# Performance work log

Measured on AMD Instinct MI355X. Metric: run time of the kernel, lower is better.

## Reference

```python
import jax, jax.numpy as jnp
import numpy as np

TEMPERATURE = 0.5
EPS = 1e-8  # matches torch cosine_similarity eps guard semantics (norm clamp)


def setup_inputs() -> dict:
    key = jax.random.key(0)
    k1, k2 = jax.random.split(key)
    B, D = 4096, 256
    z_i = jax.random.normal(k1, (B, D), dtype=jnp.float32)
    z_j = jax.random.normal(k2, (B, D), dtype=jnp.float32)
    return {"z_i": z_i, "z_j": z_j}


def reference(z_i, z_j):
    B = z_i.shape[0]
    z = jnp.concatenate([z_i, z_j], axis=0)            # [2B, D]
    # cosine similarity: normalize once, then GEMM
    norm = jnp.maximum(jnp.linalg.norm(z, axis=1, keepdims=True), EPS)
    zn = z / norm                                       # [2B, D]
    sim = zn @ zn.T                                     # [2B, 2B]
    # positives: diag(sim, +B) and diag(sim, -B)
    idx = jnp.arange(B)
    sim_ij = sim[idx, idx + B]
    sim_ji = sim[idx + B, idx]
    positives = jnp.concatenate([sim_ij, sim_ji])       # [2B]
    # masked denominator: exclude self-similarity
    mask = 1.0 - jnp.eye(2 * B, dtype=sim.dtype)
    denom = jnp.sum(mask * jnp.exp(sim / TEMPERATURE), axis=1)  # [2B]
    all_losses = -jnp.log(jnp.exp(positives / TEMPERATURE) / denom)
    return jnp.sum(all_losses) / (2 * B)
```

## Files before the change

### kernel.cpp

```cpp
#include <hip/hip_runtime.h>
#include <hip/hip_bf16.h>
#include <cstdint>
#include <cstddef>
#include <math.h>

#define D 256
#define TEMP_INV 2.0f
#define EPS_NORM 1e-8f
#define NTILES 2080

typedef __attribute__((ext_vector_type(8))) short bf16x8;
typedef __attribute__((ext_vector_type(4))) float f32x4;

__global__ void __launch_bounds__(256) normalize_rows(
    const float* __restrict__ zi, const float* __restrict__ zj,
    __hip_bfloat16* __restrict__ zn, float* __restrict__ out, int B) {
  const int wid = threadIdx.x >> 6;
  const int lane = threadIdx.x & 63;
  if (blockIdx.x == 0 && threadIdx.x == 0) out[0] = 0.0f;
#pragma unroll
  for (int it = 0; it < 4; ++it) {
    int row = it * 2048 + blockIdx.x * 4 + wid;
    const float* src = (row < B) ? (zi + (size_t)row * D)
                                 : (zj + (size_t)(row - B) * D);
    float4 v = ((const float4*)src)[lane];
    float ss = v.x * v.x + v.y * v.y + v.z * v.z + v.w * v.w;
    for (int off = 32; off; off >>= 1) ss += __shfl_xor(ss, off);
    float rn = 1.0f / fmaxf(sqrtf(ss), EPS_NORM);
    union { ushort4 u; __hip_bfloat16 h[4]; } o;
    o.h[0] = __float2bfloat16(v.x * rn);
    o.h[1] = __float2bfloat16(v.y * rn);
    o.h[2] = __float2bfloat16(v.z * rn);
    o.h[3] = __float2bfloat16(v.w * rn);
    ((ushort4*)zn)[(size_t)row * (D / 4) + lane] = o.u;
  }
}

__device__ __forceinline__ void decode_tile(int t, int Nb, int& by, int& bx) {
  float fb = (2.0f * Nb + 1.0f -
              sqrtf((float)((2 * Nb + 1) * (2 * Nb + 1) - 8 * t))) * 0.5f;
  int y = (int)fb;
  while ((y + 1) * Nb - ((y + 1) * y) / 2 <= t) ++y;
  while (y * Nb - (y * (y - 1)) / 2 > t) --y;
  by = y;
  bx = y + (t - (y * Nb - (y * (y - 1)) / 2));
}

__global__ void __launch_bounds__(256, 4) ntxent_gemm(
    const __hip_bfloat16* __restrict__ zn,
    float* __restrict__ part, float* __restrict__ pos, int B) {
  __shared__ __align__(16) __hip_bfloat16 Ash[128 * 64];
  __shared__ __align__(16) __hip_bfloat16 Bsh[128 * 64];

  const int N = 2 * B;
  const int Nb = N / 128;
  const int t = (blockIdx.x & 7) * (NTILES / 8) + (blockIdx.x >> 3);
  int by, bx;
  decode_tile(t, Nb, by, bx);
  const int bm = by * 128;
  const int bn = bx * 128;
  const bool isDiag = (by == bx);
  const bool isPos = (bx == by + B / 128);

  const int tid = threadIdx.x;
  const int wid = tid >> 6;
  const int lane = tid & 63;
  const int wy = wid >> 1, wx = wid & 1;
  const int wrow0 = wid * 32;

  const int lr = lane >> 3;
  const int c8 = lane & 7;

  const int frow = lane & 15;
  const int quad = lane >> 4;
  const int f7 = frow & 7;

  f32x4 acc[4][4] = {};

  const __hip_bfloat16* gA = zn + (size_t)(bm + wrow0 + lr) * D + c8 * 8;
  const __hip_bfloat16* gB = zn + (size_t)(bn + wrow0 + lr) * D + c8 * 8;
  const int ldsoff = (wrow0 + lr) * 64 + (c8 ^ lr) * 8;

  float4 va0 = *(const float4*)(gA + 0 * 8 * D);
  float4 va1 = *(const float4*)(gA + 1 * 8 * D);
  float4 va2 = *(const float4*)(gA + 2 * 8 * D);
  float4 va3 = *(const float4*)(gA + 3 * 8 * D);
  float4 vb0 = *(const float4*)(gB + 0 * 8 * D);
  float4 vb1 = *(const float4*)(gB + 1 * 8 * D);
  float4 vb2 = *(const float4*)(gB + 2 * 8 * D);
  float4 vb3 = *(const float4*)(gB + 3 * 8 * D);

#pragma unroll
  for (int k0i = 0; k0i < 4; ++k0i) {
    __syncthreads();
    *(float4*)&Ash[ldsoff + 0 * 8 * 64] = va0;
    *(float4*)&Ash[ldsoff + 1 * 8 * 64] = va1;
    *(float4*)&Ash[ldsoff + 2 * 8 * 64] = va2;
    *(float4*)&Ash[ldsoff + 3 * 8 * 64] = va3;
    *(float4*)&Bsh[ldsoff + 0 * 8 * 64] = vb0;
    *(float4*)&Bsh[ldsoff + 1 * 8 * 64] = vb1;
    *(float4*)&Bsh[ldsoff + 2 * 8 * 64] = vb2;
    *(float4*)&Bsh[ldsoff + 3 * 8 * 64] = vb3;
    __syncthreads();
    if (k0i < 3) {
      const int k0 = (k0i + 1) * 64;
      va0 = *(const float4*)(gA + 0 * 8 * D + k0);
      va1 = *(const float4*)(gA + 1 * 8 * D + k0);
      va2 = *(const float4*)(gA + 2 * 8 * D + k0);
      va3 = *(const float4*)(gA + 3 * 8 * D + k0);
      vb0 = *(const float4*)(gB + 0 * 8 * D + k0);
      vb1 = *(const float4*)(gB + 1 * 8 * D + k0);
      vb2 = *(const float4*)(gB + 2 * 8 * D + k0);
      vb3 = *(const float4*)(gB + 3 * 8 * D + k0);
    }
#pragma unroll
    for (int kk = 0; kk < 2; ++kk) {
      bf16x8 a[4], b[4];
#pragma unroll
      for (int i = 0; i < 4; ++i)
        a[i] = *(const bf16x8*)
            &Ash[(wy * 64 + i * 16 + frow) * 64 + ((kk * 4 + quad) ^ f7) * 8];
#pragma unroll
      for (int j = 0; j < 4; ++j)
        b[j] = *(const bf16x8*)
            &Bsh[(wx * 64 + j * 16 + frow) * 64 + ((kk * 4 + quad) ^ f7) * 8];
#pragma unroll
      for (int i = 0; i < 4; ++i)
#pragma unroll
        for (int j = 0; j < 4; ++j)
          acc[i][j] =
              __builtin_amdgcn_mfma_f32_16x16x32_bf16(a[i], b[j], acc[i][j], 0, 0, 0);
    }
  }

  float* red = (float*)&Ash[0];

  const int colq = lane & 15;
  float cs[4] = {0.0f, 0.0f, 0.0f, 0.0f};
#pragma unroll
  for (int i = 0; i < 4; ++i) {
#pragma unroll
    for (int r = 0; r < 4; ++r) {
      int rowloc = wy * 64 + i * 16 + quad * 4 + r;
      int row = bm + rowloc;
      float rs = 0.0f;
#pragma unroll
      for (int j = 0; j < 4; ++j) {
        int col = bn + wx * 64 + j * 16 + colq;
        float v = acc[i][j][r];
        float e = __expf(v * TEMP_INV);
        e = (isDiag && col == row) ? 0.0f : e;
        rs += e;
        cs[j] += e;
        if (isPos && col == row + B) { pos[row] = v; pos[col] = v; }
      }
      rs += __shfl_xor(rs, 1);
      rs += __shfl_xor(rs, 2);
      rs += __shfl_xor(rs, 4);
      rs += __shfl_xor(rs, 8);
      if (colq == 0) red[rowloc * 2 + wx] = rs;
    }
  }
#pragma unroll
  for (int j = 0; j < 4; ++j) {
    float c = cs[j];
    c += __shfl_xor(c, 16);
    c += __shfl_xor(c, 32);
    if (quad == 0) red[256 + (wx * 64 + j * 16 + colq) * 2 + wy] = c;
  }
  __syncthreads();
  if (tid < 128) {
    part[(size_t)bx * N + bm + tid] = red[tid * 2] + red[tid * 2 + 1];
  } else if (!isDiag) {
    int tt = tid - 128;
    part[(size_t)by * N + bn + tt] = red[256 + tt * 2] + red[256 + tt * 2 + 1];
  }
}

__global__ void __launch_bounds__(256) finalize(
    const float* __restrict__ part, const float* __restrict__ pos,
    float* __restrict__ out, int N) {
  const int idx = blockIdx.x * 256 + threadIdx.x;
  const int NS = N / 128;
  float s = 0.0f;
#pragma unroll 8
  for (int k = 0; k < NS; ++k) s += part[(size_t)k * N + idx];
  float loss = __logf(s) - pos[idx] * TEMP_INV;
  for (int off = 32; off; off >>= 1) loss += __shfl_xor(loss, off);
  __shared__ float redsh[4];
  if ((threadIdx.x & 63) == 0) redsh[threadIdx.x >> 6] = loss;
  __syncthreads();
  if (threadIdx.x == 0) {
    float tt = redsh[0] + redsh[1] + redsh[2] + redsh[3];
    atomicAdd(out, tt / (float)N);
  }
}

extern "C" void kernel_launch(void* const* d_in, const int* in_sizes, int n_in,
                              void* d_out, int out_size, void* d_ws, size_t ws_size,
                              hipStream_t stream) {
  const float* zi = (const float*)d_in[0];
  const float* zj = (const float*)d_in[1];
  const int B = in_sizes[0] / D;
  const int N = 2 * B;

  __hip_bfloat16* zn = (__hip_bfloat16*)d_ws;
  float* pos = (float*)((char*)d_ws + (size_t)N * D * sizeof(__hip_bfloat16));
  float* part = pos + N;

  normalize_rows<<<512, 256, 0, stream>>>(zi, zj, zn, (float*)d_out, B);
  ntxent_gemm<<<NTILES, 256, 0, stream>>>(zn, part, pos, B);
  finalize<<<N / 256, 256, 0, stream>>>(part, pos, (float*)d_out, N);
}
```

Baseline: 99.21 us.

## Make triangular-tile GEMM persistent with an atomic work queue and cross-tile prefetch

```diff
diff --git a/kernel.cpp b/kernel.cpp
--- a/kernel.cpp
+++ b/kernel.cpp
@@ -8,16 +8,21 @@
 #define TEMP_INV 2.0f
 #define EPS_NORM 1e-8f
 #define NTILES 2080
+#define GEMM_GRID 1024
 
 typedef __attribute__((ext_vector_type(8))) short bf16x8;
 typedef __attribute__((ext_vector_type(4))) float f32x4;
 
 __global__ void __launch_bounds__(256) normalize_rows(
     const float* __restrict__ zi, const float* __restrict__ zj,
-    __hip_bfloat16* __restrict__ zn, float* __restrict__ out, int B) {
+    __hip_bfloat16* __restrict__ zn, float* __restrict__ out,
+    int* __restrict__ queue, int B) {
   const int wid = threadIdx.x >> 6;
   const int lane = threadIdx.x & 63;
-  if (blockIdx.x == 0 && threadIdx.x == 0) out[0] = 0.0f;
+  if (blockIdx.x == 0 && threadIdx.x == 0) {
+    out[0] = 0.0f;
+    queue[0] = GEMM_GRID;
+  }
 #pragma unroll
   for (int it = 0; it < 4; ++it) {
     int row = it * 2048 + blockIdx.x * 4 + wid;
@@ -48,19 +53,14 @@
 
 __global__ void __launch_bounds__(256, 4) ntxent_gemm(
     const __hip_bfloat16* __restrict__ zn,
-    float* __restrict__ part, float* __restrict__ pos, int B) {
+    float* __restrict__ part, float* __restrict__ pos,
+    int* __restrict__ queue, int B) {
   __shared__ __align__(16) __hip_bfloat16 Ash[128 * 64];
   __shared__ __align__(16) __hip_bfloat16 Bsh[128 * 64];
+  __shared__ int nextT_sh;
 
   const int N = 2 * B;
   const int Nb = N / 128;
-  const int t = (blockIdx.x & 7) * (NTILES / 8) + (blockIdx.x >> 3);
-  int by, bx;
-  decode_tile(t, Nb, by, bx);
-  const int bm = by * 128;
-  const int bn = bx * 128;
-  const bool isDiag = (by == bx);
-  const bool isPos = (bx == by + B / 128);
 
   const int tid = threadIdx.x;
   const int wid = tid >> 6;
@@ -70,16 +70,18 @@
 
   const int lr = lane >> 3;
   const int c8 = lane & 7;
-
   const int frow = lane & 15;
   const int quad = lane >> 4;
   const int f7 = frow & 7;
-
-  f32x4 acc[4][4] = {};
-
-  const __hip_bfloat16* gA = zn + (size_t)(bm + wrow0 + lr) * D + c8 * 8;
-  const __hip_bfloat16* gB = zn + (size_t)(bn + wrow0 + lr) * D + c8 * 8;
   const int ldsoff = (wrow0 + lr) * 64 + (c8 ^ lr) * 8;
+  const int stageoff = (wrow0 + lr) * D + c8 * 8;
+
+  int by, bx;
+  decode_tile(blockIdx.x, Nb, by, bx);
+  int bm = by * 128, bn = bx * 128;
+
+  const __hip_bfloat16* gA = zn + (size_t)bm * D + stageoff;
+  const __hip_bfloat16* gB = zn + (size_t)bn * D + stageoff;
 
   float4 va0 = *(const float4*)(gA + 0 * 8 * D);
   float4 va1 = *(const float4*)(gA + 1 * 8 * D);
@@ -90,90 +92,119 @@
   float4 vb2 = *(const float4*)(gB + 2 * 8 * D);
   float4 vb3 = *(const float4*)(gB + 3 * 8 * D);
 
-#pragma unroll
-  for (int k0i = 0; k0i < 4; ++k0i) {
+  while (true) {
+    const bool isDiag = (by == bx);
+    const bool isPos = (bx == by + B / 128);
+    f32x4 acc[4][4] = {};
+    int nt = 0, byN = 0, bxN = 0;
+
+#pragma unroll
+    for (int k0i = 0; k0i < 4; ++k0i) {
+      if (k0i == 0 && tid == 0) nextT_sh = atomicAdd(queue, 1);
+      __syncthreads();
+      *(float4*)&Ash[ldsoff + 0 * 8 * 64] = va0;
+      *(float4*)&Ash[ldsoff + 1 * 8 * 64] = va1;
+      *(float4*)&Ash[ldsoff + 2 * 8 * 64] = va2;
+      *(float4*)&Ash[ldsoff + 3 * 8 * 64] = va3;
+      *(float4*)&Bsh[ldsoff + 0 * 8 * 64] = vb0;
+      *(float4*)&Bsh[ldsoff + 1 * 8 * 64] = vb1;
+      *(float4*)&Bsh[ldsoff + 2 * 8 * 64] = vb2;
+      *(float4*)&Bsh[ldsoff + 3 * 8 * 64] = vb3;
+      __syncthreads();
+      if (k0i == 2) {
+        nt = nextT_sh;
+        int ntc = (nt < NTILES) ? nt : 0;
+        decode_tile(ntc, Nb, byN, bxN);
+      }
+      if (k0i < 3) {
+        const int k0 = (k0i + 1) * 64;
+        va0 = *(const float4*)(gA + 0 * 8 * D + k0);
+        va1 = *(const float4*)(gA + 1 * 8 * D + k0);
+        va2 = *(const float4*)(gA + 2 * 8 * D + k0);
+        va3 = *(const float4*)(gA + 3 * 8 * D + k0);
+        vb0 = *(const float4*)(gB + 0 * 8 * D + k0);
+        vb1 = *(const float4*)(gB + 1 * 8 * D + k0);
+        vb2 = *(const float4*)(gB + 2 * 8 * D + k0);
+        vb3 = *(const float4*)(gB + 3 * 8 * D + k0);
+      } else {
+        gA = zn + (size_t)(byN * 128) * D + stageoff;
+        gB = zn + (size_t)(bxN * 128) * D + stageoff;
+        va0 = *(const float4*)(gA + 0 * 8 * D);
+        va1 = *(const float4*)(gA + 1 * 8 * D);
+        va2 = *(const float4*)(gA + 2 * 8 * D);
+        va3 = *(const float4*)(gA + 3 * 8 * D);
+        vb0 = *(const float4*)(gB + 0 * 8 * D);
+        vb1 = *(const float4*)(gB + 1 * 8 * D);
+        vb2 = *(const float4*)(gB + 2 * 8 * D);
+        vb3 = *(const float4*)(gB + 3 * 8 * D);
+      }
+#pragma unroll
+      for (int kk = 0; kk < 2; ++kk) {
+        bf16x8 a[4], b[4];
+#pragma unroll
+        for (int i = 0; i < 4; ++i)
+          a[i] = *(const bf16x8*)
+              &Ash[(wy * 64 + i * 16 + frow) * 64 + ((kk * 4 + quad) ^ f7) * 8];
+#pragma unroll
+        for (int j = 0; j < 4; ++j)
+          b[j] = *(const bf16x8*)
+              &Bsh[(wx * 64 + j * 16 + frow) * 64 + ((kk * 4 + quad) ^ f7) * 8];
+#pragma unroll
+        for (int i = 0; i < 4; ++i)
+#pragma unroll
+          for (int j = 0; j < 4; ++j)
+            acc[i][j] = __builtin_amdgcn_mfma_f32_16x16x32_bf16(
+                a[i], b[j], acc[i][j], 0, 0, 0);
+      }
+    }
+
     __syncthreads();
-    *(float4*)&Ash[ldsoff + 0 * 8 * 64] = va0;
-    *(float4*)&Ash[ldsoff + 1 * 8 * 64] = va1;
-    *(float4*)&Ash[ldsoff + 2 * 8 * 64] = va2;
-    *(float4*)&Ash[ldsoff + 3 * 8 * 64] = va3;
-    *(float4*)&Bsh[ldsoff + 0 * 8 * 64] = vb0;
-    *(float4*)&Bsh[ldsoff + 1 * 8 * 64] = vb1;
-    *(float4*)&Bsh[ldsoff + 2 * 8 * 64] = vb2;
-    *(float4*)&Bsh[ldsoff + 3 * 8 * 64] = vb3;
+    float* red = (float*)&Ash[0];
+    const int colq = lane & 15;
+    float cs[4] = {0.0f, 0.0f, 0.0f, 0.0f};
+#pragma unroll
+    for (int i = 0; i < 4; ++i) {
+#pragma unroll
+      for (int r = 0; r < 4; ++r) {
+        int rowloc = wy * 64 + i * 16 + quad * 4 + r;
+        int row = bm + rowloc;
+        float rs = 0.0f;
+#pragma unroll
+        for (int j = 0; j < 4; ++j) {
+          int col = bn + wx * 64 + j * 16 + colq;
+          float v = acc[i][j][r];
+          float e = __expf(v * TEMP_INV);
+          e = (isDiag && col == row) ? 0.0f : e;
+          rs += e;
+          cs[j] += e;
+          if (isPos && col == row + B) { pos[row] = v; pos[col] = v; }
+        }
+        rs += __shfl_xor(rs, 1);
+        rs += __shfl_xor(rs, 2);
+        rs += __shfl_xor(rs, 4);
+        rs += __shfl_xor(rs, 8);
+        if (colq == 0) red[rowloc * 2 + wx] = rs;
+      }
+    }
+#pragma unroll
+    for (int j = 0; j < 4; ++j) {
+      float c = cs[j];
+      c += __shfl_xor(c, 16);
+      c += __shfl_xor(c, 32);
+      if (quad == 0) red[256 + (wx * 64 + j * 16 + colq) * 2 + wy] = c;
+    }
     __syncthreads();
-    if (k0i < 3) {
-      const int k0 = (k0i + 1) * 64;
-      va0 = *(const float4*)(gA + 0 * 8 * D + k0);
-      va1 = *(const float4*)(gA + 1 * 8 * D + k0);
-      va2 = *(const float4*)(gA + 2 * 8 * D + k0);
-      va3 = *(const float4*)(gA + 3 * 8 * D + k0);
-      vb0 = *(const float4*)(gB + 0 * 8 * D + k0);
-      vb1 = *(const float4*)(gB + 1 * 8 * D + k0);
-      vb2 = *(const float4*)(gB + 2 * 8 * D + k0);
-      vb3 = *(const float4*)(gB + 3 * 8 * D + k0);
-    }
-#pragma unroll
-    for (int kk = 0; kk < 2; ++kk) {
-      bf16x8 a[4], b[4];
-#pragma unroll
-      for (int i = 0; i < 4; ++i)
-        a[i] = *(const bf16x8*)
-            &Ash[(wy * 64 + i * 16 + frow) * 64 + ((kk * 4 + quad) ^ f7) * 8];
-#pragma unroll
-      for (int j = 0; j < 4; ++j)
-        b[j] = *(const bf16x8*)
-            &Bsh[(wx * 64 + j * 16 + frow) * 64 + ((kk * 4 + quad) ^ f7) * 8];
-#pragma unroll
-      for (int i = 0; i < 4; ++i)
-#pragma unroll
-        for (int j = 0; j < 4; ++j)
-          acc[i][j] =
-              __builtin_amdgcn_mfma_f32_16x16x32_bf16(a[i], b[j], acc[i][j], 0, 0, 0);
-    }
-  }
-
-  float* red = (float*)&Ash[0];
-
-  const int colq = lane & 15;
-  float cs[4] = {0.0f, 0.0f, 0.0f, 0.0f};
-#pragma unroll
-  for (int i = 0; i < 4; ++i) {
-#pragma unroll
-    for (int r = 0; r < 4; ++r) {
-      int rowloc = wy * 64 + i * 16 + quad * 4 + r;
-      int row = bm + rowloc;
-      float rs = 0.0f;
-#pragma unroll
-      for (int j = 0; j < 4; ++j) {
-        int col = bn + wx * 64 + j * 16 + colq;
-        float v = acc[i][j][r];
-        float e = __expf(v * TEMP_INV);
-        e = (isDiag && col == row) ? 0.0f : e;
-        rs += e;
-        cs[j] += e;
-        if (isPos && col == row + B) { pos[row] = v; pos[col] = v; }
-      }
-      rs += __shfl_xor(rs, 1);
-      rs += __shfl_xor(rs, 2);
-      rs += __shfl_xor(rs, 4);
-      rs += __shfl_xor(rs, 8);
-      if (colq == 0) red[rowloc * 2 + wx] = rs;
-    }
-  }
-#pragma unroll
-  for (int j = 0; j < 4; ++j) {
-    float c = cs[j];
-    c += __shfl_xor(c, 16);
-    c += __shfl_xor(c, 32);
-    if (quad == 0) red[256 + (wx * 64 + j * 16 + colq) * 2 + wy] = c;
-  }
-  __syncthreads();
-  if (tid < 128) {
-    part[(size_t)bx * N + bm + tid] = red[tid * 2] + red[tid * 2 + 1];
-  } else if (!isDiag) {
-    int tt = tid - 128;
-    part[(size_t)by * N + bn + tt] = red[256 + tt * 2] + red[256 + tt * 2 + 1];
+    if (tid < 128) {
+      part[(size_t)bx * N + bm + tid] = red[tid * 2] + red[tid * 2 + 1];
+    } else if (!isDiag) {
+      int tt = tid - 128;
+      part[(size_t)by * N + bn + tt] =
+          red[256 + tt * 2] + red[256 + tt * 2 + 1];
+    }
+
+    if (nt >= NTILES) break;
+    by = byN; bx = bxN;
+    bm = byN * 128; bn = bxN * 128;
   }
 }
 
@@ -207,8 +238,9 @@
   __hip_bfloat16* zn = (__hip_bfloat16*)d_ws;
   float* pos = (float*)((char*)d_ws + (size_t)N * D * sizeof(__hip_bfloat16));
   float* part = pos + N;
-
-  normalize_rows<<<512, 256, 0, stream>>>(zi, zj, zn, (float*)d_out, B);
-  ntxent_gemm<<<NTILES, 256, 0, stream>>>(zn, part, pos, B);
+  int* queue = (int*)(part + (size_t)(N / 128) * N);
+
+  normalize_rows<<<512, 256, 0, stream>>>(zi, zj, zn, (float*)d_out, queue, B);
+  ntxent_gemm<<<GEMM_GRID, 256, 0, stream>>>(zn, part, pos, queue, B);
   finalize<<<N / 256, 256, 0, stream>>>(part, pos, (float*)d_out, N);
 }
```

After: 153.3 us. +54.5%, slower.
